# Performance work log

Hardware: AMD Instinct MI355X
Metric: run time of the kernel (lower is better)

## Reference

```python
import jax, jax.numpy as jnp
import numpy as np

COORD_W, EDGE_W, COUNT_W, REG_W, CONTRA_W = 1.0, 2.0, 0.1, 0.001, 0.1
MARGIN = 1.0


def setup_inputs() -> dict:
    key = jax.random.key(0)
    ks = jax.random.split(key, 6)
    B, N, D, C = 16, 1024, 128, 2
    return {
        "predicted_coords": jax.random.normal(ks[0], (B, N, C), jnp.float32),
        "points": jax.random.normal(ks[1], (B, N, C), jnp.float32),
        "adjacency_logits": jax.random.normal(ks[2], (B, N, N), jnp.float32),
        "adjacency": jax.random.bernoulli(ks[3], 0.1, (B, N, N)).astype(jnp.float32),
        "node_masks": jnp.ones((B, N), jnp.float32),  # all nodes valid -> n_actual = N
        "predicted_count": jax.random.normal(ks[4], (B, 1), jnp.float32),
        "node_features": jax.random.normal(ks[5], (B, N, D), jnp.float32),
    }


def _bce_with_logits(logits, targets):
    # mean-reduced, numerically stable (matches F.binary_cross_entropy_with_logits)
    return jnp.mean(jnp.maximum(logits, 0.0) - logits * targets
                    + jnp.log1p(jnp.exp(-jnp.abs(logits))))


def _smooth_l1(pred, target):
    d = jnp.abs(pred - target)
    return jnp.mean(jnp.where(d < 1.0, 0.5 * d * d, d - 0.5))


def _contrastive_sample(features, adj):
    # features: [N, D], adj: [N, N]. torch.cdist pairwise euclidean via gram trick.
    nrm = jnp.sum(features * features, axis=-1)              # [N]
    sq = jnp.maximum(nrm[:, None] + nrm[None, :]
                     - 2.0 * (features @ features.T), 0.0)   # [N, N] squared dists
    n = features.shape[0]
    eye = jnp.eye(n, dtype=bool)
    pos_mask = adj > 0.5
    neg_mask = (adj <= 0.5) & (~eye)
    # positive term: mean of distances**2 over positive pairs == mean squared dist
    pos = jnp.sum(jnp.where(pos_mask, sq, 0.0)) / jnp.maximum(jnp.sum(pos_mask), 1)
    dist = jnp.sqrt(jnp.maximum(sq, 1e-12))
    hinge = jnp.square(jax.nn.relu(MARGIN - dist))
    neg = jnp.sum(jnp.where(neg_mask, hinge, 0.0)) / jnp.maximum(jnp.sum(neg_mask), 1)
    return pos + neg


def reference(predicted_coords, points, adjacency_logits, adjacency,
              node_masks, predicted_count, node_features):
    # node_masks are all ones, so the per-sample [:n_actual] slicing is the
    # full tensor; per-sample MSE/BCE means averaged over batch equal global means.
    coord_loss = jnp.mean(jnp.square(predicted_coords - points))
    edge_loss = _bce_with_logits(adjacency_logits, adjacency)
    actual_counts = jnp.sum(node_masks, axis=1)              # [B]
    count_loss = _smooth_l1(predicted_count[:, 0], actual_counts)
    reg_loss = jnp.mean(jnp.square(node_features))
    # contrastive path uses targets['adjacency'] (no predicted_adjacency key)
    contra_loss = jnp.mean(jax.vmap(_contrastive_sample)(node_features, adjacency))
    total = (COORD_W * coord_loss + EDGE_W * edge_loss + COUNT_W * count_loss
             + REG_W * reg_loss + CONTRA_W * contra_loss)
    return total, coord_loss, edge_loss, count_loss, reg_loss, contra_loss
```

## Files before the change

kernel.cpp:

```cpp
#include <hip/hip_runtime.h>
#include <hip/hip_bf16.h>

#define NN    1024
#define DD    128
#define TILE  128
#define PITCH 136
#define SQP   132

typedef __bf16 bf16_t;
typedef bf16_t bf16x8 __attribute__((ext_vector_type(8)));
typedef float  f32x4  __attribute__((ext_vector_type(4)));


__global__ __launch_bounds__(256) void small_losses(
    const float* __restrict__ pcoord, const float* __restrict__ pts,
    const float* __restrict__ masks,  const float* __restrict__ pcount,
    float* __restrict__ ws) {
  __shared__ float sh[4][2];
  float coord = 0.f, cnt = 0.f;

  const int gt = blockIdx.x * 256 + threadIdx.x;
  const int stride = 16 * 256;

  const float4* a4 = (const float4*)pcoord;
  const float4* b4 = (const float4*)pts;
  for (int i = gt; i < 8192; i += stride) {
    float4 a = a4[i], b = b4[i];
    float dx = a.x-b.x, dy = a.y-b.y, dz = a.z-b.z, dw = a.w-b.w;
    coord += dx*dx + dy*dy + dz*dz + dw*dw;
  }
  const float* m = masks + blockIdx.x * NN;
  for (int i = threadIdx.x; i < NN; i += 256) cnt += m[i];

  const int lane = threadIdx.x & 63, w = threadIdx.x >> 6;
  #pragma unroll
  for (int o = 32; o; o >>= 1) {
    coord += __shfl_xor(coord, o);
    cnt   += __shfl_xor(cnt, o);
  }
  if (lane == 0) { sh[w][0] = coord; sh[w][1] = cnt; }
  __syncthreads();
  if (threadIdx.x == 0) {
    float c = 0.f, n = 0.f;
    for (int i = 0; i < 4; ++i) { c += sh[i][0]; n += sh[i][1]; }
    atomicAdd(&ws[0], c);
    float d = fabsf(pcount[blockIdx.x] - n);
    float term = (d < 1.f) ? 0.5f * d * d : d - 0.5f;
    atomicAdd(&ws[2], term);
  }
}

__device__ __forceinline__ void loss_elem(float l, float a, float s, int grow, int gcol,
    float& bsum, float& poss, float& posc, float& negs, float& negc) {
  bsum += fmaxf(l, 0.f) - l * a + __logf(1.f + __expf(-fabsf(l)));
  if (a > 0.5f) {
    poss += s; posc += 1.f;
  } else if (grow != gcol) {
    negc += 1.f;
    if (s < 1.f) {
      float d = sqrtf(fmaxf(s, 1e-12f));
      float h = 1.f - d;
      negs += h * h;
    }
  }
}

__global__ __launch_bounds__(512, 4) void fused_gram_bce(
    const float* __restrict__ logits, const float* __restrict__ adj,
    const float* __restrict__ feat, float* __restrict__ ws) {
  __shared__ __align__(16) char smem[2 * TILE * PITCH * sizeof(bf16_t)];
  bf16_t* lsA = (bf16_t*)smem;
  bf16_t* lsB = (bf16_t*)(smem + TILE * PITCH * sizeof(bf16_t));
  float*  sqb = (float*)smem;
  __shared__ float nrmA[TILE];
  __shared__ float nrmB[TILE];
  __shared__ float red[8][6];

  const int bx  = blockIdx.x;
  const int b   = bx >> 6;
  const int tid = bx & 63;
  const int ti  = (tid >> 3) << 7;
  const int tj  = (tid & 7)  << 7;
  const bool diag = (ti == tj);

  const int t = threadIdx.x;
  const float* fb = feat + (size_t)b * NN * DD;

  float regsum = 0.f;
  #pragma unroll
  for (int it = 0; it < 8; ++it) {
    int cid  = it * 512 + t;
    int tile = cid >> 11;
    int sub  = cid & 2047;
    int row  = sub >> 4;
    int c8   = sub & 15;
    const float* src = fb + (size_t)((tile ? tj : ti) + row) * DD + c8 * 8;
    float4 u = *(const float4*)src;
    float4 v = *(const float4*)(src + 4);
    if (diag && tile == 0)
      regsum += u.x*u.x + u.y*u.y + u.z*u.z + u.w*u.w
              + v.x*v.x + v.y*v.y + v.z*v.z + v.w*v.w;
    bf16_t* dst = (tile ? lsB : lsA) + row * PITCH + c8 * 8;
    dst[0] = (bf16_t)u.x; dst[1] = (bf16_t)u.y; dst[2] = (bf16_t)u.z; dst[3] = (bf16_t)u.w;
    dst[4] = (bf16_t)v.x; dst[5] = (bf16_t)v.y; dst[6] = (bf16_t)v.z; dst[7] = (bf16_t)v.w;
  }
  __syncthreads();

  {
    int row  = t >> 1;
    int half = t & 1;
    const bf16_t* src = (row < 128 ? lsA + row * PITCH : lsB + (row - 128) * PITCH)
                        + half * 64;
    float s = 0.f;
    #pragma unroll
    for (int c = 0; c < 8; ++c) {
      bf16x8 ch = *(const bf16x8*)(src + c * 8);
      #pragma unroll
      for (int i = 0; i < 8; ++i) { float v = (float)ch[i]; s += v * v; }
    }
    s += __shfl_xor(s, 1);
    if (half == 0) {
      if (row < 128) nrmA[row] = s; else nrmB[row - 128] = s;
    }
  }
  __syncthreads();

  const int lane = t & 63;
  const int wave = t >> 6;
  const int lrow = lane & 15;
  const int quad = lane >> 4;

  f32x4 acc[8];
  #pragma unroll
  for (int fc = 0; fc < 8; ++fc) acc[fc] = (f32x4){0.f, 0.f, 0.f, 0.f};

  #pragma unroll
  for (int k0 = 0; k0 < DD; k0 += 32) {
    const int kc = k0 + quad * 8;
    bf16x8 aF = *(const bf16x8*)&lsA[(wave * 16 + lrow) * PITCH + kc];
    bf16x8 bF[8];
    #pragma unroll
    for (int fc = 0; fc < 8; ++fc)
      bF[fc] = *(const bf16x8*)&lsB[(fc * 16 + lrow) * PITCH + kc];
    #pragma unroll
    for (int fc = 0; fc < 8; ++fc)
      acc[fc] = __builtin_amdgcn_mfma_f32_16x16x32_bf16(aF, bF[fc], acc[fc], 0, 0, 0);
  }
  __syncthreads();

  {
    const int rbase = wave * 16 + quad * 4;
    #pragma unroll
    for (int fc = 0; fc < 8; ++fc) {
      const int ctile = fc * 16 + lrow;
      const float ncol = nrmB[ctile];
      #pragma unroll
      for (int r = 0; r < 4; ++r) {
        const int rtile = rbase + r;
        sqb[rtile * SQP + ctile] = fmaxf(nrmA[rtile] + ncol - 2.f * acc[fc][r], 0.f);
      }
    }
  }
  __syncthreads();

  float bsum = 0.f, poss = 0.f, posc = 0.f, negs = 0.f, negc = 0.f;
  const size_t base = (size_t)b * NN * NN;
  const int c4 = t & 31, r0 = t >> 5;
  const int gcol0 = tj + c4 * 4;
  const float* lp = logits + base + (size_t)(ti + r0) * NN + gcol0;
  const float* ap = adj    + base + (size_t)(ti + r0) * NN + gcol0;

  float4 l0 = *(const float4*)lp;
  float4 a0 = *(const float4*)ap;
  #pragma unroll
  for (int it = 0; it < 8; ++it) {
    float4 l = l0, a = a0;
    if (it < 7) {
      l0 = *(const float4*)(lp + (size_t)(it + 1) * 16 * NN);
      a0 = *(const float4*)(ap + (size_t)(it + 1) * 16 * NN);
    }
    const int row  = it * 16 + r0;
    const int grow = ti + row;
    float4 s = *(const float4*)&sqb[row * SQP + c4 * 4];
    loss_elem(l.x, a.x, s.x, grow, gcol0 + 0, bsum, poss, posc, negs, negc);
    loss_elem(l.y, a.y, s.y, grow, gcol0 + 1, bsum, poss, posc, negs, negc);
    loss_elem(l.z, a.z, s.z, grow, gcol0 + 2, bsum, poss, posc, negs, negc);
    loss_elem(l.w, a.w, s.w, grow, gcol0 + 3, bsum, poss, posc, negs, negc);
  }

  #pragma unroll
  for (int o = 32; o; o >>= 1) {
    bsum   += __shfl_xor(bsum, o);
    poss   += __shfl_xor(poss, o);
    posc   += __shfl_xor(posc, o);
    negs   += __shfl_xor(negs, o);
    negc   += __shfl_xor(negc, o);
    regsum += __shfl_xor(regsum, o);
  }
  if (lane == 0) {
    red[wave][0] = bsum; red[wave][1] = poss; red[wave][2] = posc;
    red[wave][3] = negs; red[wave][4] = negc; red[wave][5] = regsum;
  }
  __syncthreads();
  if (t == 0) {
    float s0 = 0.f, s1 = 0.f, s2 = 0.f, s3 = 0.f, s4 = 0.f, s5 = 0.f;
    for (int w = 0; w < 8; ++w) {
      s0 += red[w][0]; s1 += red[w][1]; s2 += red[w][2];
      s3 += red[w][3]; s4 += red[w][4]; s5 += red[w][5];
    }
    atomicAdd(&ws[3], s0);
    atomicAdd(&ws[4 + b], s1);
    atomicAdd(&ws[20 + b], s2);
    atomicAdd(&ws[36 + b], s3);
    atomicAdd(&ws[52 + b], s4);
    if (diag) atomicAdd(&ws[1], s5);
  }
}

__global__ void finalize(const float* __restrict__ ws, float* __restrict__ out) {
  if (threadIdx.x != 0 || blockIdx.x != 0) return;
  float coord = ws[0] / 32768.f;
  float reg   = ws[1] / 2097152.f;
  float cntl  = ws[2] / 16.f;
  float edge  = ws[3] / 16777216.f;
  float contra = 0.f;
  for (int b = 0; b < 16; ++b) {
    float p = ws[4 + b]  / fmaxf(ws[20 + b], 1.f);
    float n = ws[36 + b] / fmaxf(ws[52 + b], 1.f);
    contra += p + n;
  }
  contra *= (1.f / 16.f);
  float total = coord + 2.f * edge + 0.1f * cntl + 0.001f * reg + 0.1f * contra;
  out[0] = total; out[1] = coord; out[2] = edge;
  out[3] = cntl;  out[4] = reg;   out[5] = contra;
}

extern "C" void kernel_launch(void* const* d_in, const int* in_sizes, int n_in,
                              void* d_out, int out_size, void* d_ws, size_t ws_size,
                              hipStream_t stream) {
  (void)in_sizes; (void)n_in; (void)out_size; (void)ws_size;
  const float* pcoord = (const float*)d_in[0];
  const float* pts    = (const float*)d_in[1];
  const float* logits = (const float*)d_in[2];
  const float* adj    = (const float*)d_in[3];
  const float* masks  = (const float*)d_in[4];
  const float* pcount = (const float*)d_in[5];
  const float* nf     = (const float*)d_in[6];
  float* ws  = (float*)d_ws;
  float* out = (float*)d_out;

  hipMemsetAsync(ws, 0, 68 * sizeof(float), stream);
  small_losses<<<16, 256, 0, stream>>>(pcoord, pts, masks, pcount, ws);
  fused_gram_bce<<<1024, 512, 0, stream>>>(logits, adj, nf, ws);
  finalize<<<1, 64, 0, stream>>>(ws, out);
}
```

Before: 200.6 us.

## Fuse all losses into one kernel with 64x64 tiles and last-block finalize

Merges the small-loss kernel and the finalize kernel into the main gram/BCE kernel: the per-batch tile 0 block computes the coord and count losses, and the last block to finish, found through an atomic counter, writes the outputs. Tiles shrink from 128x128 to 64x64, which quadruples the block count and raises the occupancy hint to 6 so more waves can hide the streaming of the logits and adjacency. Feature rows are reloaded more often as a result, and the extra global atomics add traffic.

```diff
diff --git a/kernel.cpp b/kernel.cpp
--- a/kernel.cpp
+++ b/kernel.cpp
@@ -3,52 +3,15 @@
 
 #define NN    1024
 #define DD    128
-#define TILE  128
+#define BT    64
 #define PITCH 136
-#define SQP   132
+#define SQP   68
+#define NBLK  4096
 
 typedef __bf16 bf16_t;
 typedef bf16_t bf16x8 __attribute__((ext_vector_type(8)));
 typedef float  f32x4  __attribute__((ext_vector_type(4)));
 
-
-__global__ __launch_bounds__(256) void small_losses(
-    const float* __restrict__ pcoord, const float* __restrict__ pts,
-    const float* __restrict__ masks,  const float* __restrict__ pcount,
-    float* __restrict__ ws) {
-  __shared__ float sh[4][2];
-  float coord = 0.f, cnt = 0.f;
-
-  const int gt = blockIdx.x * 256 + threadIdx.x;
-  const int stride = 16 * 256;
-
-  const float4* a4 = (const float4*)pcoord;
-  const float4* b4 = (const float4*)pts;
-  for (int i = gt; i < 8192; i += stride) {
-    float4 a = a4[i], b = b4[i];
-    float dx = a.x-b.x, dy = a.y-b.y, dz = a.z-b.z, dw = a.w-b.w;
-    coord += dx*dx + dy*dy + dz*dz + dw*dw;
-  }
-  const float* m = masks + blockIdx.x * NN;
-  for (int i = threadIdx.x; i < NN; i += 256) cnt += m[i];
-
-  const int lane = threadIdx.x & 63, w = threadIdx.x >> 6;
-  #pragma unroll
-  for (int o = 32; o; o >>= 1) {
-    coord += __shfl_xor(coord, o);
-    cnt   += __shfl_xor(cnt, o);
-  }
-  if (lane == 0) { sh[w][0] = coord; sh[w][1] = cnt; }
-  __syncthreads();
-  if (threadIdx.x == 0) {
-    float c = 0.f, n = 0.f;
-    for (int i = 0; i < 4; ++i) { c += sh[i][0]; n += sh[i][1]; }
-    atomicAdd(&ws[0], c);
-    float d = fabsf(pcount[blockIdx.x] - n);
-    float term = (d < 1.f) ? 0.5f * d * d : d - 0.5f;
-    atomicAdd(&ws[2], term);
-  }
-}
 
 __device__ __forceinline__ void loss_elem(float l, float a, float s, int grow, int gcol,
     float& bsum, float& poss, float& posc, float& negs, float& negc) {
@@ -65,33 +28,47 @@
   }
 }
 
-__global__ __launch_bounds__(512, 4) void fused_gram_bce(
+__global__ __launch_bounds__(512, 6) void fused_all(
     const float* __restrict__ logits, const float* __restrict__ adj,
-    const float* __restrict__ feat, float* __restrict__ ws) {
-  __shared__ __align__(16) char smem[2 * TILE * PITCH * sizeof(bf16_t)];
+    const float* __restrict__ feat,   const float* __restrict__ pcoord,
+    const float* __restrict__ pts,    const float* __restrict__ masks,
+    const float* __restrict__ pcount, float* __restrict__ ws,
+    float* __restrict__ out) {
+  __shared__ __align__(16) char smem[2 * BT * PITCH * sizeof(bf16_t)];
   bf16_t* lsA = (bf16_t*)smem;
-  bf16_t* lsB = (bf16_t*)(smem + TILE * PITCH * sizeof(bf16_t));
+  bf16_t* lsB = (bf16_t*)(smem + BT * PITCH * sizeof(bf16_t));
   float*  sqb = (float*)smem;
-  __shared__ float nrmA[TILE];
-  __shared__ float nrmB[TILE];
-  __shared__ float red[8][6];
+  __shared__ float nrmA[BT], nrmB[BT];
+  __shared__ float red[8][8];
 
   const int bx  = blockIdx.x;
-  const int b   = bx >> 6;
-  const int tid = bx & 63;
-  const int ti  = (tid >> 3) << 7;
-  const int tj  = (tid & 7)  << 7;
-  const bool diag = (ti == tj);
+  const int b   = bx >> 8;
+  const int tid = bx & 255;
+  const int ti  = (tid >> 4) << 6;
+  const int tj  = (tid & 15) << 6;
+  const bool diag    = (ti == tj);
+  const bool special = (tid == 0);
 
   const int t = threadIdx.x;
   const float* fb = feat + (size_t)b * NN * DD;
 
+  float coordsum = 0.f, cntsum = 0.f;
+  if (special) {
+    const float4* a4 = (const float4*)(pcoord + (size_t)b * NN * 2);
+    const float4* b4 = (const float4*)(pts    + (size_t)b * NN * 2);
+    float4 ac = a4[t], bc = b4[t];
+    float dx = ac.x-bc.x, dy = ac.y-bc.y, dz = ac.z-bc.z, dw = ac.w-bc.w;
+    coordsum = dx*dx + dy*dy + dz*dz + dw*dw;
+    const float* m = masks + b * NN;
+    cntsum = m[t] + m[t + 512];
+  }
+
   float regsum = 0.f;
   #pragma unroll
-  for (int it = 0; it < 8; ++it) {
+  for (int it = 0; it < 4; ++it) {
     int cid  = it * 512 + t;
-    int tile = cid >> 11;
-    int sub  = cid & 2047;
+    int tile = cid >> 10;
+    int sub  = cid & 1023;
     int row  = sub >> 4;
     int c8   = sub & 15;
     const float* src = fb + (size_t)((tile ? tj : ti) + row) * DD + c8 * 8;
@@ -107,132 +84,141 @@
   __syncthreads();
 
   {
-    int row  = t >> 1;
-    int half = t & 1;
-    const bf16_t* src = (row < 128 ? lsA + row * PITCH : lsB + (row - 128) * PITCH)
-                        + half * 64;
+    int row = t >> 2;
+    int q   = t & 3;
+    const bf16_t* src = (row < BT ? lsA + row * PITCH : lsB + (row - BT) * PITCH)
+                        + q * 32;
     float s = 0.f;
     #pragma unroll
-    for (int c = 0; c < 8; ++c) {
+    for (int c = 0; c < 4; ++c) {
       bf16x8 ch = *(const bf16x8*)(src + c * 8);
       #pragma unroll
       for (int i = 0; i < 8; ++i) { float v = (float)ch[i]; s += v * v; }
     }
     s += __shfl_xor(s, 1);
-    if (half == 0) {
-      if (row < 128) nrmA[row] = s; else nrmB[row - 128] = s;
-    }
-  }
-  __syncthreads();
+    s += __shfl_xor(s, 2);
+    if (q == 0) { if (row < BT) nrmA[row] = s; else nrmB[row - BT] = s; }
+  }
 
   const int lane = t & 63;
   const int wave = t >> 6;
   const int lrow = lane & 15;
   const int quad = lane >> 4;
-
-  f32x4 acc[8];
-  #pragma unroll
-  for (int fc = 0; fc < 8; ++fc) acc[fc] = (f32x4){0.f, 0.f, 0.f, 0.f};
-
+  const int rf = wave >> 1;
+  const int h  = wave & 1;
+
+  f32x4 acc[2];
+  acc[0] = (f32x4){0.f,0.f,0.f,0.f};
+  acc[1] = (f32x4){0.f,0.f,0.f,0.f};
   #pragma unroll
   for (int k0 = 0; k0 < DD; k0 += 32) {
     const int kc = k0 + quad * 8;
-    bf16x8 aF = *(const bf16x8*)&lsA[(wave * 16 + lrow) * PITCH + kc];
-    bf16x8 bF[8];
+    bf16x8 aF = *(const bf16x8*)&lsA[(rf * 16 + lrow) * PITCH + kc];
     #pragma unroll
-    for (int fc = 0; fc < 8; ++fc)
-      bF[fc] = *(const bf16x8*)&lsB[(fc * 16 + lrow) * PITCH + kc];
+    for (int c = 0; c < 2; ++c) {
+      bf16x8 bF = *(const bf16x8*)&lsB[((h * 2 + c) * 16 + lrow) * PITCH + kc];
+      acc[c] = __builtin_amdgcn_mfma_f32_16x16x32_bf16(aF, bF, acc[c], 0, 0, 0);
+    }
+  }
+  __syncthreads();
+
+  {
+    const int rbase = rf * 16 + quad * 4;
     #pragma unroll
-    for (int fc = 0; fc < 8; ++fc)
-      acc[fc] = __builtin_amdgcn_mfma_f32_16x16x32_bf16(aF, bF[fc], acc[fc], 0, 0, 0);
-  }
-  __syncthreads();
-
-  {
-    const int rbase = wave * 16 + quad * 4;
-    #pragma unroll
-    for (int fc = 0; fc < 8; ++fc) {
-      const int ctile = fc * 16 + lrow;
+    for (int c = 0; c < 2; ++c) {
+      const int ctile = (h * 2 + c) * 16 + lrow;
       const float ncol = nrmB[ctile];
       #pragma unroll
-      for (int r = 0; r < 4; ++r) {
-        const int rtile = rbase + r;
-        sqb[rtile * SQP + ctile] = fmaxf(nrmA[rtile] + ncol - 2.f * acc[fc][r], 0.f);
-      }
+      for (int r = 0; r < 4; ++r)
+        sqb[(rbase + r) * SQP + ctile] =
+            fmaxf(nrmA[rbase + r] + ncol - 2.f * acc[c][r], 0.f);
     }
   }
   __syncthreads();
 
   float bsum = 0.f, poss = 0.f, posc = 0.f, negs = 0.f, negc = 0.f;
   const size_t base = (size_t)b * NN * NN;
-  const int c4 = t & 31, r0 = t >> 5;
+  const int c4 = t & 15, r0 = t >> 4;
   const int gcol0 = tj + c4 * 4;
   const float* lp = logits + base + (size_t)(ti + r0) * NN + gcol0;
   const float* ap = adj    + base + (size_t)(ti + r0) * NN + gcol0;
-
-  float4 l0 = *(const float4*)lp;
-  float4 a0 = *(const float4*)ap;
-  #pragma unroll
-  for (int it = 0; it < 8; ++it) {
-    float4 l = l0, a = a0;
-    if (it < 7) {
-      l0 = *(const float4*)(lp + (size_t)(it + 1) * 16 * NN);
-      a0 = *(const float4*)(ap + (size_t)(it + 1) * 16 * NN);
-    }
-    const int row  = it * 16 + r0;
-    const int grow = ti + row;
-    float4 s = *(const float4*)&sqb[row * SQP + c4 * 4];
-    loss_elem(l.x, a.x, s.x, grow, gcol0 + 0, bsum, poss, posc, negs, negc);
-    loss_elem(l.y, a.y, s.y, grow, gcol0 + 1, bsum, poss, posc, negs, negc);
-    loss_elem(l.z, a.z, s.z, grow, gcol0 + 2, bsum, poss, posc, negs, negc);
-    loss_elem(l.w, a.w, s.w, grow, gcol0 + 3, bsum, poss, posc, negs, negc);
+  float4 L0 = *(const float4*)lp;
+  float4 A0 = *(const float4*)ap;
+  float4 L1 = *(const float4*)(lp + (size_t)32 * NN);
+  float4 A1 = *(const float4*)(ap + (size_t)32 * NN);
+  float4 s0 = *(const float4*)&sqb[r0 * SQP + c4 * 4];
+  float4 s1 = *(const float4*)&sqb[(r0 + 32) * SQP + c4 * 4];
+  {
+    int grow = ti + r0;
+    loss_elem(L0.x, A0.x, s0.x, grow, gcol0 + 0, bsum, poss, posc, negs, negc);
+    loss_elem(L0.y, A0.y, s0.y, grow, gcol0 + 1, bsum, poss, posc, negs, negc);
+    loss_elem(L0.z, A0.z, s0.z, grow, gcol0 + 2, bsum, poss, posc, negs, negc);
+    loss_elem(L0.w, A0.w, s0.w, grow, gcol0 + 3, bsum, poss, posc, negs, negc);
+    grow += 32;
+    loss_elem(L1.x, A1.x, s1.x, grow, gcol0 + 0, bsum, poss, posc, negs, negc);
+    loss_elem(L1.y, A1.y, s1.y, grow, gcol0 + 1, bsum, poss, posc, negs, negc);
+    loss_elem(L1.z, A1.z, s1.z, grow, gcol0 + 2, bsum, poss, posc, negs, negc);
+    loss_elem(L1.w, A1.w, s1.w, grow, gcol0 + 3, bsum, poss, posc, negs, negc);
   }
 
   #pragma unroll
   for (int o = 32; o; o >>= 1) {
-    bsum   += __shfl_xor(bsum, o);
-    poss   += __shfl_xor(poss, o);
-    posc   += __shfl_xor(posc, o);
-    negs   += __shfl_xor(negs, o);
-    negc   += __shfl_xor(negc, o);
-    regsum += __shfl_xor(regsum, o);
+    bsum     += __shfl_xor(bsum, o);
+    poss     += __shfl_xor(poss, o);
+    posc     += __shfl_xor(posc, o);
+    negs     += __shfl_xor(negs, o);
+    negc     += __shfl_xor(negc, o);
+    regsum   += __shfl_xor(regsum, o);
+    coordsum += __shfl_xor(coordsum, o);
+    cntsum   += __shfl_xor(cntsum, o);
   }
   if (lane == 0) {
-    red[wave][0] = bsum; red[wave][1] = poss; red[wave][2] = posc;
-    red[wave][3] = negs; red[wave][4] = negc; red[wave][5] = regsum;
+    red[wave][0] = bsum;   red[wave][1] = poss;     red[wave][2] = posc;
+    red[wave][3] = negs;   red[wave][4] = negc;     red[wave][5] = regsum;
+    red[wave][6] = coordsum; red[wave][7] = cntsum;
   }
   __syncthreads();
   if (t == 0) {
-    float s0 = 0.f, s1 = 0.f, s2 = 0.f, s3 = 0.f, s4 = 0.f, s5 = 0.f;
+    float s0_=0.f,s1_=0.f,s2_=0.f,s3_=0.f,s4_=0.f,s5_=0.f,s6_=0.f,s7_=0.f;
     for (int w = 0; w < 8; ++w) {
-      s0 += red[w][0]; s1 += red[w][1]; s2 += red[w][2];
-      s3 += red[w][3]; s4 += red[w][4]; s5 += red[w][5];
-    }
-    atomicAdd(&ws[3], s0);
-    atomicAdd(&ws[4 + b], s1);
-    atomicAdd(&ws[20 + b], s2);
-    atomicAdd(&ws[36 + b], s3);
-    atomicAdd(&ws[52 + b], s4);
-    if (diag) atomicAdd(&ws[1], s5);
-  }
-}
-
-__global__ void finalize(const float* __restrict__ ws, float* __restrict__ out) {
-  if (threadIdx.x != 0 || blockIdx.x != 0) return;
-  float coord = ws[0] / 32768.f;
-  float reg   = ws[1] / 2097152.f;
-  float cntl  = ws[2] / 16.f;
-  float edge  = ws[3] / 16777216.f;
-  float contra = 0.f;
-  for (int b = 0; b < 16; ++b) {
-    float p = ws[4 + b]  / fmaxf(ws[20 + b], 1.f);
-    float n = ws[36 + b] / fmaxf(ws[52 + b], 1.f);
-    contra += p + n;
-  }
-  contra *= (1.f / 16.f);
-  float total = coord + 2.f * edge + 0.1f * cntl + 0.001f * reg + 0.1f * contra;
-  out[0] = total; out[1] = coord; out[2] = edge;
-  out[3] = cntl;  out[4] = reg;   out[5] = contra;
+      s0_ += red[w][0]; s1_ += red[w][1]; s2_ += red[w][2]; s3_ += red[w][3];
+      s4_ += red[w][4]; s5_ += red[w][5]; s6_ += red[w][6]; s7_ += red[w][7];
+    }
+    atomicAdd(&ws[3], s0_);
+    atomicAdd(&ws[4 + b], s1_);
+    atomicAdd(&ws[20 + b], s2_);
+    atomicAdd(&ws[36 + b], s3_);
+    atomicAdd(&ws[52 + b], s4_);
+    if (diag) atomicAdd(&ws[1], s5_);
+    if (special) {
+      atomicAdd(&ws[0], s6_);
+      float d = fabsf(pcount[b] - s7_);
+      float term = (d < 1.f) ? 0.5f * d * d : d - 0.5f;
+      atomicAdd(&ws[2], term);
+    }
+    __threadfence();
+    unsigned old = atomicAdd((unsigned*)(ws + 68), 1u);
+    if (old == NBLK - 1) {
+      __threadfence();
+      float v[68];
+      for (int i = 0; i < 68; ++i)
+        v[i] = __hip_atomic_load(&ws[i], __ATOMIC_RELAXED, __HIP_MEMORY_SCOPE_AGENT);
+      float coord = v[0] / 32768.f;
+      float reg   = v[1] / 2097152.f;
+      float cntl  = v[2] / 16.f;
+      float edge  = v[3] / 16777216.f;
+      float contra = 0.f;
+      for (int bb = 0; bb < 16; ++bb) {
+        float p = v[4 + bb]  / fmaxf(v[20 + bb], 1.f);
+        float n = v[36 + bb] / fmaxf(v[52 + bb], 1.f);
+        contra += p + n;
+      }
+      contra *= (1.f / 16.f);
+      float total = coord + 2.f*edge + 0.1f*cntl + 0.001f*reg + 0.1f*contra;
+      out[0] = total; out[1] = coord; out[2] = edge;
+      out[3] = cntl;  out[4] = reg;   out[5] = contra;
+    }
+  }
 }
 
 extern "C" void kernel_launch(void* const* d_in, const int* in_sizes, int n_in,
@@ -249,8 +235,7 @@
   float* ws  = (float*)d_ws;
   float* out = (float*)d_out;
 
-  hipMemsetAsync(ws, 0, 68 * sizeof(float), stream);
-  small_losses<<<16, 256, 0, stream>>>(pcoord, pts, masks, pcount, ws);
-  fused_gram_bce<<<1024, 512, 0, stream>>>(logits, adj, nf, ws);
-  finalize<<<1, 64, 0, stream>>>(ws, out);
+  hipMemsetAsync(ws, 0, 69 * sizeof(float), stream);
+  fused_all<<<NBLK, 512, 0, stream>>>(logits, adj, nf, pcoord, pts, masks,
+                                      pcount, ws, out);
 }
```

After: 368.3 us. 1.84x slower.

## Shrink row tile to 64 and launch twice as many blocks for more occupancy

Applied to the files above, without the earlier changes.

Changes the fused Gram/BCE kernel from 128x128 to 64x128 output tiles, doubling the grid to 2048 blocks. LDS use and per-wave accumulators shrink, and launch bounds rise to 6 blocks per SM so more waves are resident to hide the memory-bound logits/adjacency streaming. It also drops one barrier after the norm computation and issues the first logits/adjacency loads before the sq-tile barrier so they overlap. In exchange, each block reloads the 128-row B feature tile for fewer output rows, adding redundant feature traffic and bf16 conversion, and the register sum is now taken by the tj==0 blocks.

```diff
diff --git a/kernel.cpp b/kernel.cpp
--- a/kernel.cpp
+++ b/kernel.cpp
@@ -3,9 +3,11 @@
 
 #define NN    1024
 #define DD    128
-#define TILE  128
+#define AR    64
+#define BR    128
 #define PITCH 136
 #define SQP   132
+#define NBLK  2048
 
 typedef __bf16 bf16_t;
 typedef bf16_t bf16x8 __attribute__((ext_vector_type(8)));
@@ -65,51 +67,50 @@
   }
 }
 
-__global__ __launch_bounds__(512, 4) void fused_gram_bce(
+__global__ __launch_bounds__(512, 6) void fused_gram_bce(
     const float* __restrict__ logits, const float* __restrict__ adj,
     const float* __restrict__ feat, float* __restrict__ ws) {
-  __shared__ __align__(16) char smem[2 * TILE * PITCH * sizeof(bf16_t)];
+  __shared__ __align__(16) char smem[(AR + BR) * PITCH * sizeof(bf16_t)];
   bf16_t* lsA = (bf16_t*)smem;
-  bf16_t* lsB = (bf16_t*)(smem + TILE * PITCH * sizeof(bf16_t));
+  bf16_t* lsB = (bf16_t*)(smem + AR * PITCH * sizeof(bf16_t));
   float*  sqb = (float*)smem;
-  __shared__ float nrmA[TILE];
-  __shared__ float nrmB[TILE];
+  __shared__ float nrmA[AR], nrmB[BR];
   __shared__ float red[8][6];
 
   const int bx  = blockIdx.x;
-  const int b   = bx >> 6;
-  const int tid = bx & 63;
-  const int ti  = (tid >> 3) << 7;
+  const int b   = bx >> 7;
+  const int tid = bx & 127;
+  const int ti  = (tid >> 3) << 6;
   const int tj  = (tid & 7)  << 7;
-  const bool diag = (ti == tj);
+  const bool regblk = ((tid & 7) == 0);
 
   const int t = threadIdx.x;
   const float* fb = feat + (size_t)b * NN * DD;
 
   float regsum = 0.f;
   #pragma unroll
-  for (int it = 0; it < 8; ++it) {
+  for (int it = 0; it < 6; ++it) {
     int cid  = it * 512 + t;
-    int tile = cid >> 11;
-    int sub  = cid & 2047;
-    int row  = sub >> 4;
-    int c8   = sub & 15;
-    const float* src = fb + (size_t)((tile ? tj : ti) + row) * DD + c8 * 8;
+    int row  = cid >> 4;
+    int c8   = cid & 15;
+    const bool isA = row < AR;
+    const int grow = isA ? (ti + row) : (tj + row - AR);
+    const float* src = fb + (size_t)grow * DD + c8 * 8;
     float4 u = *(const float4*)src;
     float4 v = *(const float4*)(src + 4);
-    if (diag && tile == 0)
+    if (regblk && isA)
       regsum += u.x*u.x + u.y*u.y + u.z*u.z + u.w*u.w
               + v.x*v.x + v.y*v.y + v.z*v.z + v.w*v.w;
-    bf16_t* dst = (tile ? lsB : lsA) + row * PITCH + c8 * 8;
+    bf16_t* dst = (isA ? lsA + row * PITCH : lsB + (row - AR) * PITCH) + c8 * 8;
     dst[0] = (bf16_t)u.x; dst[1] = (bf16_t)u.y; dst[2] = (bf16_t)u.z; dst[3] = (bf16_t)u.w;
     dst[4] = (bf16_t)v.x; dst[5] = (bf16_t)v.y; dst[6] = (bf16_t)v.z; dst[7] = (bf16_t)v.w;
   }
   __syncthreads();
 
-  {
+  if (t < 384) {
     int row  = t >> 1;
     int half = t & 1;
-    const bf16_t* src = (row < 128 ? lsA + row * PITCH : lsB + (row - 128) * PITCH)
+    const bf16_t* src = (row < AR ? lsA + row * PITCH : lsB + (row - AR) * PITCH)
                         + half * 64;
     float s = 0.f;
     #pragma unroll
@@ -119,40 +120,46 @@
       for (int i = 0; i < 8; ++i) { float v = (float)ch[i]; s += v * v; }
     }
     s += __shfl_xor(s, 1);
-    if (half == 0) {
-      if (row < 128) nrmA[row] = s; else nrmB[row - 128] = s;
-    }
-  }
-  __syncthreads();
+    if (half == 0) { if (row < AR) nrmA[row] = s; else nrmB[row - AR] = s; }
+  }
 
   const int lane = t & 63;
   const int wave = t >> 6;
   const int lrow = lane & 15;
   const int quad = lane >> 4;
-
-  f32x4 acc[8];
-  #pragma unroll
-  for (int fc = 0; fc < 8; ++fc) acc[fc] = (f32x4){0.f, 0.f, 0.f, 0.f};
+  const int rf = wave >> 1;
+  const int h  = wave & 1;
+
+  f32x4 acc[4];
+  #pragma unroll
+  for (int fc = 0; fc < 4; ++fc) acc[fc] = (f32x4){0.f, 0.f, 0.f, 0.f};
 
   #pragma unroll
   for (int k0 = 0; k0 < DD; k0 += 32) {
     const int kc = k0 + quad * 8;
-    bf16x8 aF = *(const bf16x8*)&lsA[(wave * 16 + lrow) * PITCH + kc];
-    bf16x8 bF[8];
+    bf16x8 aF = *(const bf16x8*)&lsA[(rf * 16 + lrow) * PITCH + kc];
     #pragma unroll
-    for (int fc = 0; fc < 8; ++fc)
-      bF[fc] = *(const bf16x8*)&lsB[(fc * 16 + lrow) * PITCH + kc];
+    for (int fc = 0; fc < 4; ++fc) {
+      bf16x8 bF = *(const bf16x8*)&lsB[((h * 4 + fc) * 16 + lrow) * PITCH + kc];
+      acc[fc] = __builtin_amdgcn_mfma_f32_16x16x32_bf16(aF, bF, acc[fc], 0, 0, 0);
+    }
+  }
+
+  const int c4 = t & 31, r0 = t >> 5;
+  const int gcol0 = tj + c4 * 4;
+  const size_t base = (size_t)b * NN * NN;
+  const float* lp = logits + base + (size_t)(ti + r0) * NN + gcol0;
+  const float* ap = adj    + base + (size_t)(ti + r0) * NN + gcol0;
+  float4 L0 = *(const float4*)lp;
+  float4 A0 = *(const float4*)ap;
+
+  __syncthreads();
+
+  {
+    const int rbase = rf * 16 + quad * 4;
     #pragma unroll
-    for (int fc = 0; fc < 8; ++fc)
-      acc[fc] = __builtin_amdgcn_mfma_f32_16x16x32_bf16(aF, bF[fc], acc[fc], 0, 0, 0);
-  }
-  __syncthreads();
-
-  {
-    const int rbase = wave * 16 + quad * 4;
-    #pragma unroll
-    for (int fc = 0; fc < 8; ++fc) {
-      const int ctile = fc * 16 + lrow;
+    for (int fc = 0; fc < 4; ++fc) {
+      const int ctile = (h * 4 + fc) * 16 + lrow;
       const float ncol = nrmB[ctile];
       #pragma unroll
       for (int r = 0; r < 4; ++r) {
@@ -164,28 +171,20 @@
   __syncthreads();
 
   float bsum = 0.f, poss = 0.f, posc = 0.f, negs = 0.f, negc = 0.f;
-  const size_t base = (size_t)b * NN * NN;
-  const int c4 = t & 31, r0 = t >> 5;
-  const int gcol0 = tj + c4 * 4;
-  const float* lp = logits + base + (size_t)(ti + r0) * NN + gcol0;
-  const float* ap = adj    + base + (size_t)(ti + r0) * NN + gcol0;
-
-  float4 l0 = *(const float4*)lp;
-  float4 a0 = *(const float4*)ap;
-  #pragma unroll
-  for (int it = 0; it < 8; ++it) {
-    float4 l = l0, a = a0;
-    if (it < 7) {
-      l0 = *(const float4*)(lp + (size_t)(it + 1) * 16 * NN);
-      a0 = *(const float4*)(ap + (size_t)(it + 1) * 16 * NN);
+  #pragma unroll
+  for (int it = 0; it < 4; ++it) {
+    float4 L = L0, A = A0;
+    if (it < 3) {
+      L0 = *(const float4*)(lp + (size_t)(it + 1) * 16 * NN);
+      A0 = *(const float4*)(ap + (size_t)(it + 1) * 16 * NN);
     }
     const int row  = it * 16 + r0;
     const int grow = ti + row;
     float4 s = *(const float4*)&sqb[row * SQP + c4 * 4];
-    loss_elem(l.x, a.x, s.x, grow, gcol0 + 0, bsum, poss, posc, negs, negc);
-    loss_elem(l.y, a.y, s.y, grow, gcol0 + 1, bsum, poss, posc, negs, negc);
-    loss_elem(l.z, a.z, s.z, grow, gcol0 + 2, bsum, poss, posc, negs, negc);
-    loss_elem(l.w, a.w, s.w, grow, gcol0 + 3, bsum, poss, posc, negs, negc);
+    loss_elem(L.x, A.x, s.x, grow, gcol0 + 0, bsum, poss, posc, negs, negc);
+    loss_elem(L.y, A.y, s.y, grow, gcol0 + 1, bsum, poss, posc, negs, negc);
+    loss_elem(L.z, A.z, s.z, grow, gcol0 + 2, bsum, poss, posc, negs, negc);
+    loss_elem(L.w, A.w, s.w, grow, gcol0 + 3, bsum, poss, posc, negs, negc);
   }
 
   #pragma unroll
@@ -203,7 +202,7 @@
   }
   __syncthreads();
   if (t == 0) {
-    float s0 = 0.f, s1 = 0.f, s2 = 0.f, s3 = 0.f, s4 = 0.f, s5 = 0.f;
+    float s0=0.f,s1=0.f,s2=0.f,s3=0.f,s4=0.f,s5=0.f;
     for (int w = 0; w < 8; ++w) {
       s0 += red[w][0]; s1 += red[w][1]; s2 += red[w][2];
       s3 += red[w][3]; s4 += red[w][4]; s5 += red[w][5];
@@ -213,7 +212,7 @@
     atomicAdd(&ws[20 + b], s2);
     atomicAdd(&ws[36 + b], s3);
     atomicAdd(&ws[52 + b], s4);
-    if (diag) atomicAdd(&ws[1], s5);
+    if (regblk) atomicAdd(&ws[1], s5);
   }
 }
 
@@ -251,6 +250,6 @@
 
   hipMemsetAsync(ws, 0, 68 * sizeof(float), stream);
   small_losses<<<16, 256, 0, stream>>>(pcoord, pts, masks, pcount, ws);
-  fused_gram_bce<<<1024, 512, 0, stream>>>(logits, adj, nf, ws);
+  fused_gram_bce<<<NBLK, 512, 0, stream>>>(logits, adj, nf, ws);
   finalize<<<1, 64, 0, stream>>>(ws, out);
 }
```

After: 212.3 us. +5.9%, slower.
